# Kernel optimization log

Hardware: AMD Instinct MI355X
Metric: run time of the kernel (lower is better)

Reference implementation:

```python
import jax, jax.numpy as jnp
import numpy as np

DIM = 512
HEADS = 8
DIM_HEAD = 64
HIDDEN = HEADS * DIM_HEAD  # 512
SCALE = DIM_HEAD ** -0.5
EPS = 1e-12  # F.normalize default eps


def rms_norm(x, g):
    # F.normalize over channel dim (dim=1), then * g * sqrt(C)
    c = x.shape[1]
    norm = jnp.sqrt(jnp.sum(x * x, axis=1, keepdims=True))
    return x / jnp.maximum(norm, EPS) * g * (c ** 0.5)


def setup_inputs() -> dict:
    key = jax.random.key(0)
    ks = jax.random.split(key, 6)
    b, h, w = 16, 64, 64
    x = jax.random.normal(ks[0], (b, DIM, h, w), dtype=jnp.float32)
    g1 = jnp.ones((1, DIM, 1, 1), dtype=jnp.float32)
    # 1x1 conv weights stored as (out_ch, in_ch)
    Wqkv = jax.random.normal(ks[1], (HIDDEN * 3, DIM), dtype=jnp.float32) * (DIM ** -0.5)
    Wout = jax.random.normal(ks[2], (DIM, HIDDEN), dtype=jnp.float32) * (HIDDEN ** -0.5)
    bout = jax.random.normal(ks[3], (DIM,), dtype=jnp.float32) * 0.01
    g2 = jnp.ones((1, DIM, 1, 1), dtype=jnp.float32)
    return {"x": x, "g1": g1, "Wqkv": Wqkv, "Wout": Wout, "bout": bout, "g2": g2}


def reference(x, g1, Wqkv, Wout, bout, g2):
    b, c, h, w = x.shape
    n = h * w
    xn = rms_norm(x, g1)
    # 1x1 conv == channel matmul
    qkv = jnp.einsum('oc,bchw->bohw', Wqkv, xn)  # (b, 3*hidden, h, w)
    qkv = qkv.reshape(b, 3, HEADS, DIM_HEAD, n)
    q, k, v = qkv[:, 0], qkv[:, 1], qkv[:, 2]  # (b, heads, d, n)
    q = jax.nn.softmax(q, axis=-2) * SCALE      # softmax over feature dim
    k = jax.nn.softmax(k, axis=-1)               # softmax over spatial dim
    context = jnp.einsum('bhdn,bhen->bhde', k, v)  # (b,h,d,e) small
    out = jnp.einsum('bhde,bhdn->bhen', context, q)  # (b,h,e,n)
    out = out.reshape(b, HIDDEN, h, w)
    out = jnp.einsum('oc,bchw->bohw', Wout, out) + bout[None, :, None, None]
    return rms_norm(out, g2)
```

## Files before the change

kernel.cpp:

```cpp
#include <hip/hip_runtime.h>
#include <hip/hip_bf16.h>
#include <math.h>

#define B_ 16
#define C_ 512
#define N_ 4096
#define NCOL (B_ * N_)

typedef short bf16x8 __attribute__((ext_vector_type(8)));
typedef ushort ushort8_t __attribute__((ext_vector_type(8)));
typedef float f32x4 __attribute__((ext_vector_type(4)));

__device__ __forceinline__ ushort f2bf(float f) {
    unsigned u = __float_as_uint(f);
    unsigned r = (u + 0x7FFFu + ((u >> 16) & 1u)) >> 16;
    return (ushort)r;
}
__device__ __forceinline__ float bf2f(ushort u) {
    return __uint_as_float((unsigned)u << 16);
}
__device__ __forceinline__ void gload_lds16(const void* g, void* l) {
    __builtin_amdgcn_global_load_lds(
        (const __attribute__((address_space(1))) unsigned int*)g,
        (__attribute__((address_space(3))) unsigned int*)l, 16, 0, 0);
}

__global__ __launch_bounds__(256) void wprep2_k(const float* __restrict__ Wqkv,
                                                const float* __restrict__ g1,
                                                const float* __restrict__ Wout,
                                                ushort* __restrict__ Wqkvb,
                                                ushort* __restrict__ Woutb)
{
    int i = blockIdx.x * 256 + threadIdx.x;
    if (i < 196608) {
        float4 wv = reinterpret_cast<const float4*>(Wqkv)[i];
        const float4 gv = *reinterpret_cast<const float4*>(g1 + ((i * 4) & 511));
        ushort4 u;
        u.x = f2bf(wv.x * gv.x); u.y = f2bf(wv.y * gv.y);
        u.z = f2bf(wv.z * gv.z); u.w = f2bf(wv.w * gv.w);
        reinterpret_cast<ushort4*>(Wqkvb)[i] = u;
    } else {
        int j = i - 196608;
        float4 wv = reinterpret_cast<const float4*>(Wout)[j];
        ushort4 u;
        u.x = f2bf(wv.x); u.y = f2bf(wv.y); u.z = f2bf(wv.z); u.w = f2bf(wv.w);
        reinterpret_cast<ushort4*>(Woutb)[j] = u;
    }
}

__global__ __launch_bounds__(256) void transpose_k(const float* __restrict__ X,
                                                   ushort* __restrict__ Xt,
                                                   float* __restrict__ rs1)
{
    __shared__ float t[2][64][68];
    __shared__ float sr[16][64];
    const int b = blockIdx.y, n0 = blockIdx.x * 64;
    const int tid = threadIdx.x;
    const int tg = tid >> 4, tl = tid & 15;
    float sq[4] = {0.f, 0.f, 0.f, 0.f};
    for (int chunk = 0; chunk < 8; ++chunk) {
        const int buf = chunk & 1;
        const float* xp = X + ((size_t)b * C_ + chunk * 64) * N_ + n0;
        #pragma unroll
        for (int j = 0; j < 4; ++j) {
            int c = tg + j * 16;
            float4 v = *reinterpret_cast<const float4*>(xp + (size_t)c * N_ + tl * 4);
            *reinterpret_cast<float4*>(&t[buf][c][tl * 4]) = v;
            sq[0] += v.x * v.x; sq[1] += v.y * v.y;
            sq[2] += v.z * v.z; sq[3] += v.w * v.w;
        }
        __syncthreads();
        #pragma unroll
        for (int i = 0; i < 4; ++i) {
            int nl = tg + i * 16, cl = tl * 4;
            ushort4 u;
            u.x = f2bf(t[buf][cl + 0][nl]);
            u.y = f2bf(t[buf][cl + 1][nl]);
            u.z = f2bf(t[buf][cl + 2][nl]);
            u.w = f2bf(t[buf][cl + 3][nl]);
            *reinterpret_cast<ushort4*>(
                Xt + ((size_t)b * N_ + n0 + nl) * 512 + chunk * 64 + cl) = u;
        }
    }
    #pragma unroll
    for (int j = 0; j < 4; ++j) sr[tg][tl * 4 + j] = sq[j];
    __syncthreads();
    if (tid < 64) {
        float s = 0.f;
        #pragma unroll
        for (int g = 0; g < 16; ++g) s += sr[g][tid];
        rs1[(size_t)b * N_ + n0 + tid] = 22.627416998f / fmaxf(sqrtf(s), 1e-12f);
    }
}

__global__ __launch_bounds__(512, 2)
void mfma_gemm(const ushort* __restrict__ A, const ushort* __restrict__ Bt,
               const float* __restrict__ rs1,
               ushort* __restrict__ qT2, ushort* __restrict__ kd,
               ushort* __restrict__ vd)
{
    __shared__ __align__(16) char lds[2][2][32768];
    const int b  = blockIdx.z;
    const int n0 = blockIdx.x * 256;
    const int m0 = blockIdx.y * 256;
    const int tid = threadIdx.x;
    const int w = tid >> 6, l = tid & 63;
    const int wm = w >> 2, wn = w & 3;
    const int lq = l >> 4, lr = l & 15;
    const ushort* Bb = Bt + (size_t)b * N_ * 512;

    f32x4 acc[8][4];
    #pragma unroll
    for (int i = 0; i < 8; ++i)
        #pragma unroll
        for (int j = 0; j < 4; ++j)
            #pragma unroll
            for (int r = 0; r < 4; ++r) acc[i][j][r] = 0.f;

#define STAGE_STEP(t, i)                                                      \
    do {                                                                      \
        const int kb_ = (t) * 128;                                            \
        const int idx_ = (i) * 512 + tid;                                     \
        const int r_ = idx_ >> 3;                                             \
        const int ch_ = (idx_ & 7) ^ (r_ & 7);                                \
        gload_lds16((const char*)A + (size_t)(m0 + r_) * 1024 + kb_ + ch_ * 16,\
                    &lds[(t) & 1][0][idx_ * 16]);                             \
        gload_lds16((const char*)Bb + (size_t)(n0 + r_) * 1024 + kb_ + ch_ * 16,\
                    &lds[(t) & 1][1][idx_ * 16]);                             \
    } while (0)

    #pragma unroll
    for (int i = 0; i < 4; ++i) STAGE_STEP(0, i);

    bf16x8 bfr[4];
    #pragma unroll 2
    for (int t = 0; t < 8; ++t) {
        const char* As = lds[t & 1][0];
        const char* Bs = lds[t & 1][1];
        #pragma unroll
        for (int ph = 0; ph < 4; ++ph) {
            const int kk = ph >> 1, mg = ph & 1;
            bf16x8 af[4];
            if (ph != 0) {
                #pragma unroll
                for (int m2 = 0; m2 < 4; ++m2) {
                    int ra = wm * 128 + (mg * 4 + m2) * 16 + lr;
                    int ch = (kk * 4 + lq) ^ (ra & 7);
                    af[m2] = *(const bf16x8*)(As + ra * 128 + ch * 16);
                }
                if (mg == 0) {
                    #pragma unroll
                    for (int nf = 0; nf < 4; ++nf) {
                        int rb = wn * 64 + nf * 16 + lr;
                        int ch = (kk * 4 + lq) ^ (rb & 7);
                        bfr[nf] = *(const bf16x8*)(Bs + rb * 128 + ch * 16);
                    }
                }
            }
            if (t < 7) STAGE_STEP(t + 1, ph);
            if (ph == 0) {
                if (t < 7) { asm volatile("s_waitcnt vmcnt(2)" ::: "memory"); }
                else       { asm volatile("s_waitcnt vmcnt(0)" ::: "memory"); }
            }
            __builtin_amdgcn_s_barrier();
            if (ph == 0) {
                #pragma unroll
                for (int m2 = 0; m2 < 4; ++m2) {
                    int ra = wm * 128 + m2 * 16 + lr;
                    int ch = lq ^ (ra & 7);
                    af[m2] = *(const bf16x8*)(As + ra * 128 + ch * 16);
                }
                #pragma unroll
                for (int nf = 0; nf < 4; ++nf) {
                    int rb = wn * 64 + nf * 16 + lr;
                    int ch = lq ^ (rb & 7);
                    bfr[nf] = *(const bf16x8*)(Bs + rb * 128 + ch * 16);
                }
            }
            asm volatile("s_waitcnt lgkmcnt(0)" ::: "memory");
            __builtin_amdgcn_sched_barrier(0);
            __builtin_amdgcn_s_setprio(1);
            #pragma unroll
            for (int m2 = 0; m2 < 4; ++m2)
                #pragma unroll
                for (int nf = 0; nf < 4; ++nf)
                    acc[mg * 4 + m2][nf] = __builtin_amdgcn_mfma_f32_16x16x32_bf16(
                        af[m2], bfr[nf], acc[mg * 4 + m2][nf], 0, 0, 0);
            __builtin_amdgcn_s_setprio(0);
            __builtin_amdgcn_s_barrier();
        }
    }
#undef STAGE_STEP

    const int part = m0 >> 9;
    const int mloc = (m0 & 511) + wm * 128;
    const int nbase = n0 + wn * 64;
    if (part == 0) {
        #pragma unroll
        for (int hg = 0; hg < 2; ++hg) {
            const int head = (mloc >> 6) + hg;
            #pragma unroll
            for (int nf = 0; nf < 4; ++nf) {
                const int n = nbase + nf * 16 + lr;
                const float sc = rs1[(size_t)b * N_ + n];
                float v[4][4];
                float mx = -1e30f;
                #pragma unroll
                for (int m2 = 0; m2 < 4; ++m2)
                    #pragma unroll
                    for (int r = 0; r < 4; ++r) {
                        v[m2][r] = acc[hg * 4 + m2][nf][r] * sc;
                        mx = fmaxf(mx, v[m2][r]);
                    }
                mx = fmaxf(mx, __shfl_xor(mx, 16));
                mx = fmaxf(mx, __shfl_xor(mx, 32));
                float s = 0.f;
                #pragma unroll
                for (int m2 = 0; m2 < 4; ++m2)
                    #pragma unroll
                    for (int r = 0; r < 4; ++r) {
                        v[m2][r] = __expf(v[m2][r] - mx);
                        s += v[m2][r];
                    }
                s += __shfl_xor(s, 16);
                s += __shfl_xor(s, 32);
                const float r8 = 0.125f / s;
                ushort* qp = qT2 + ((size_t)b * N_ + n) * 512 + head * 64;
                #pragma unroll
                for (int m2 = 0; m2 < 4; ++m2) {
                    ushort4 u;
                    u.x = f2bf(v[m2][0] * r8);
                    u.y = f2bf(v[m2][1] * r8);
                    u.z = f2bf(v[m2][2] * r8);
                    u.w = f2bf(v[m2][3] * r8);
                    *reinterpret_cast<ushort4*>(qp + m2 * 16 + lq * 4) = u;
                }
            }
        }
    } else {
        ushort* dst = (part == 1) ? kd : vd;
        #pragma unroll
        for (int nf = 0; nf < 4; ++nf) {
            const int n = nbase + nf * 16 + lr;
            const float sc = rs1[(size_t)b * N_ + n];
            #pragma unroll
            for (int mf = 0; mf < 8; ++mf) {
                const int o = mloc + mf * 16 + lq * 4;
                #pragma unroll
                for (int r = 0; r < 4; ++r)
                    dst[((size_t)b * 512 + o + r) * N_ + n] =
                        f2bf(acc[mf][nf][r] * sc);
            }
        }
    }
}

__global__ __launch_bounds__(256) void rowstat_k(const ushort* __restrict__ kk,
                                                 float* __restrict__ rowm,
                                                 float* __restrict__ rowr)
{
    const int row = blockIdx.x * 4 + (threadIdx.x >> 6);
    const int lane = threadIdx.x & 63;
    const ushort* p = kk + (size_t)row * N_;
    float vals[64];
    #pragma unroll
    for (int j = 0; j < 8; ++j) {
        ushort8_t u = *reinterpret_cast<const ushort8_t*>(p + lane * 8 + j * 512);
        #pragma unroll
        for (int t = 0; t < 8; ++t) vals[j * 8 + t] = bf2f(u[t]);
    }
    float mx = -1e30f;
    #pragma unroll
    for (int i = 0; i < 64; ++i) mx = fmaxf(mx, vals[i]);
    #pragma unroll
    for (int o = 32; o >= 1; o >>= 1) mx = fmaxf(mx, __shfl_xor(mx, o));
    float s = 0.f;
    #pragma unroll
    for (int i = 0; i < 64; ++i) s += __expf(vals[i] - mx);
    #pragma unroll
    for (int o = 32; o >= 1; o >>= 1) s += __shfl_xor(s, o);
    if (lane == 0) { rowm[row] = mx; rowr[row] = 1.f / s; }
}

__global__ __launch_bounds__(256) void ctx_k(const ushort* __restrict__ kk,
                                             const ushort* __restrict__ vv,
                                             const float* __restrict__ rowm,
                                             const float* __restrict__ rowr,
                                             float* __restrict__ ctxp)
{
    const int bh = blockIdx.x, chunk = blockIdx.y;
    const ushort* kp = kk + (size_t)bh * 64 * N_;
    const ushort* vp = vv + (size_t)bh * 64 * N_;
    __shared__ __align__(16) ushort kx[64 * 128];
    __shared__ __align__(16) ushort vx[64 * 128];
    __shared__ float rm[64];
    const int tid = threadIdx.x;
    const int w = tid >> 6, l = tid & 63;
    const int lq = l >> 4, lr = l & 15;
    const int we = w >> 1, wd = w & 1;
    if (tid < 64) rm[tid] = rowm[(size_t)bh * 64 + tid];
    __syncthreads();

    f32x4 acc[2][2];
    #pragma unroll
    for (int i = 0; i < 2; ++i)
        #pragma unroll
        for (int j = 0; j < 2; ++j)
            #pragma unroll
            for (int r = 0; r < 4; ++r) acc[i][j][r] = 0.f;

    for (int s = 0; s < 8; ++s) {
        const int n0 = chunk * 1024 + s * 128;
        #pragma unroll
        for (int i = 0; i < 4; ++i) {
            int idx = i * 256 + tid;
            int row = idx >> 4;
            int ch  = (idx & 15) ^ (row & 15);
            gload_lds16((const char*)(vp + (size_t)row * N_ + n0 + ch * 8),
                        (char*)vx + idx * 16);
        }
        #pragma unroll
        for (int i = 0; i < 4; ++i) {
            int idx = i * 256 + tid;
            int row = idx >> 4;
            int ch  = idx & 15;
            ushort8_t u = *reinterpret_cast<const ushort8_t*>(
                kp + (size_t)row * N_ + n0 + ch * 8);
            float m_ = rm[row];
            ushort8_t o;
            #pragma unroll
            for (int t = 0; t < 8; ++t) o[t] = f2bf(__expf(bf2f(u[t]) - m_));
            *(ushort8_t*)((char*)kx + (row * 16 + (ch ^ (row & 15))) * 16) = o;
        }
        __syncthreads();
        #pragma unroll
        for (int k2 = 0; k2 < 4; ++k2) {
            bf16x8 af[2], bfr[2];
            #pragma unroll
            for (int i = 0; i < 2; ++i) {
                int re = we * 32 + i * 16 + lr;
                int cha = (k2 * 4 + lq) ^ (re & 15);
                af[i] = *(const bf16x8*)((const char*)vx + (re * 16 + cha) * 16);
                int rd = wd * 32 + i * 16 + lr;
                int chb = (k2 * 4 + lq) ^ (rd & 15);
                bfr[i] = *(const bf16x8*)((const char*)kx + (rd * 16 + chb) * 16);
            }
            #pragma unroll
            for (int i = 0; i < 2; ++i)
                #pragma unroll
                for (int j = 0; j < 2; ++j)
                    acc[i][j] = __builtin_amdgcn_mfma_f32_16x16x32_bf16(
                        af[i], bfr[j], acc[i][j], 0, 0, 0);
        }
        __syncthreads();
    }
    float* cbase = ctxp + ((size_t)bh * 4 + chunk) * 4096;
    #pragma unroll
    for (int j = 0; j < 2; ++j) {
        const int d = wd * 32 + j * 16 + lr;
        const float rr = rowr[(size_t)bh * 64 + d];
        #pragma unroll
        for (int i = 0; i < 2; ++i) {
            const int e0 = we * 32 + i * 16 + lq * 4;
            float4 wv;
            wv.x = acc[i][j][0] * rr;
            wv.y = acc[i][j][1] * rr;
            wv.z = acc[i][j][2] * rr;
            wv.w = acc[i][j][3] * rr;
            *reinterpret_cast<float4*>(cbase + (size_t)d * 64 + e0) = wv;
        }
    }
}

__global__ __launch_bounds__(256) void wcbuild_k(const ushort* __restrict__ Wb,
                                                 const float* __restrict__ ctxp,
                                                 ushort* __restrict__ Wc)
{
    const int oh = blockIdx.x, h = blockIdx.y, b = blockIdx.z;
    const int bh = b * 8 + h;
    __shared__ __align__(16) ushort ws[256 * 64];
    __shared__ __align__(16) ushort cs[64 * 64];
    const int tid = threadIdx.x;
    const int w = tid >> 6, l = tid & 63;
    const int lq = l >> 4, lr = l & 15;

    #pragma unroll
    for (int i = 0; i < 8; ++i) {
        int idx = i * 256 + tid;
        int row = idx >> 3;
        int ch = (idx & 7) ^ (row & 7);
        gload_lds16(Wb + (size_t)(oh * 256 + row) * 512 + h * 64 + ch * 8,
                    (char*)ws + idx * 16);
    }
    {
        const float* cp = ctxp + (size_t)bh * 4 * 4096;
        const int d = tid >> 2, eb = (tid & 3) * 16;
        float vs[16];
        #pragma unroll
        for (int t4 = 0; t4 < 4; ++t4) {
            float4 a0 = *(const float4*)(cp + d * 64 + eb + t4 * 4);
            float4 a1 = *(const float4*)(cp + 4096 + d * 64 + eb + t4 * 4);
            float4 a2 = *(const float4*)(cp + 8192 + d * 64 + eb + t4 * 4);
            float4 a3 = *(const float4*)(cp + 12288 + d * 64 + eb + t4 * 4);
            vs[t4 * 4 + 0] = a0.x + a1.x + a2.x + a3.x;
            vs[t4 * 4 + 1] = a0.y + a1.y + a2.y + a3.y;
            vs[t4 * 4 + 2] = a0.z + a1.z + a2.z + a3.z;
            vs[t4 * 4 + 3] = a0.w + a1.w + a2.w + a3.w;
        }
        ushort8_t o0, o1;
        #pragma unroll
        for (int t = 0; t < 8; ++t) { o0[t] = f2bf(vs[t]); o1[t] = f2bf(vs[8 + t]); }
        const int c0 = (eb >> 3) ^ (d & 7);
        const int c1 = ((eb >> 3) + 1) ^ (d & 7);
        *(ushort8_t*)((char*)cs + (d * 8 + c0) * 16) = o0;
        *(ushort8_t*)((char*)cs + (d * 8 + c1) * 16) = o1;
    }
    __syncthreads();

    f32x4 acc[4][4];
    #pragma unroll
    for (int i = 0; i < 4; ++i)
        #pragma unroll
        for (int j = 0; j < 4; ++j)
            #pragma unroll
            for (int r = 0; r < 4; ++r) acc[i][j][r] = 0.f;

    #pragma unroll
    for (int kk = 0; kk < 2; ++kk) {
        bf16x8 af[4], bfr[4];
        #pragma unroll
        for (int mf = 0; mf < 4; ++mf) {
            int ra = w * 64 + mf * 16 + lr;
            int ch = (kk * 4 + lq) ^ (ra & 7);
            af[mf] = *(const bf16x8*)((const char*)ws + (ra * 8 + ch) * 16);
        }
        #pragma unroll
        for (int nf = 0; nf < 4; ++nf) {
            int rd = nf * 16 + lr;
            int ch = (kk * 4 + lq) ^ (rd & 7);
            bfr[nf] = *(const bf16x8*)((const char*)cs + (rd * 8 + ch) * 16);
        }
        #pragma unroll
        for (int mf = 0; mf < 4; ++mf)
            #pragma unroll
            for (int nf = 0; nf < 4; ++nf)
                acc[mf][nf] = __builtin_amdgcn_mfma_f32_16x16x32_bf16(
                    af[mf], bfr[nf], acc[mf][nf], 0, 0, 0);
    }

    ushort* wp = Wc + (size_t)b * 262144 + h * 64;
    #pragma unroll
    for (int mf = 0; mf < 4; ++mf)
        #pragma unroll
        for (int r = 0; r < 4; ++r) {
            const int o = oh * 256 + w * 64 + mf * 16 + lq * 4 + r;
            #pragma unroll
            for (int nf = 0; nf < 4; ++nf)
                wp[(size_t)o * 512 + nf * 16 + lr] = f2bf(acc[mf][nf][r]);
        }
}

__global__ __launch_bounds__(512, 2)
void gemm2_k(const ushort* __restrict__ Wc,
             const ushort* __restrict__ Bt,
             const float* __restrict__ bias,
             const float* __restrict__ g2,
             float* __restrict__ outp)
{
    __shared__ __align__(16) ushort As[512 * 64];
    __shared__ __align__(16) ushort Bs[128 * 64];
    const int b  = blockIdx.y;
    const int n0 = blockIdx.x * 128;
    const int tid = threadIdx.x;
    const int w = tid >> 6, l = tid & 63;
    const int lq = l >> 4, lr = l & 15;
    const ushort* A  = Wc + (size_t)b * 262144;
    const ushort* Bb = Bt + (size_t)b * N_ * 512;

    f32x4 acc[4][8];
    #pragma unroll
    for (int i = 0; i < 4; ++i)
        #pragma unroll
        for (int j = 0; j < 8; ++j)
            #pragma unroll
            for (int r = 0; r < 4; ++r) acc[i][j][r] = 0.f;

    for (int k0 = 0; k0 < 512; k0 += 64) {
        #pragma unroll
        for (int i = 0; i < 8; ++i) {
            int base = i * 512 + w * 64;
            int idx = base + l;
            int r = idx >> 3, ch = (idx & 7) ^ (r & 7);
            gload_lds16((const char*)A + (size_t)r * 1024 + k0 * 2 + ch * 16,
                        (char*)As + (size_t)base * 16);
        }
        #pragma unroll
        for (int i = 0; i < 2; ++i) {
            int base = i * 512 + w * 64;
            int idx = base + l;
            int r = idx >> 3, ch = (idx & 7) ^ (r & 7);
            gload_lds16((const char*)Bb + (size_t)(n0 + r) * 1024 + k0 * 2 + ch * 16,
                        (char*)Bs + (size_t)base * 16);
        }
        __syncthreads();
        #pragma unroll
        for (int kk = 0; kk < 2; ++kk) {
            bf16x8 af[4], bfv[8];
            #pragma unroll
            for (int mf = 0; mf < 4; ++mf) {
                int ra = w * 64 + mf * 16 + lr;
                int ch = (kk * 4 + lq) ^ (ra & 7);
                af[mf] = *(const bf16x8*)((const char*)As + ra * 128 + ch * 16);
            }
            #pragma unroll
            for (int nf = 0; nf < 8; ++nf) {
                int rb = nf * 16 + lr;
                int ch = (kk * 4 + lq) ^ (rb & 7);
                bfv[nf] = *(const bf16x8*)((const char*)Bs + rb * 128 + ch * 16);
            }
            #pragma unroll
            for (int mf = 0; mf < 4; ++mf)
                #pragma unroll
                for (int nf = 0; nf < 8; ++nf)
                    acc[mf][nf] = __builtin_amdgcn_mfma_f32_16x16x32_bf16(
                        af[mf], bfv[nf], acc[mf][nf], 0, 0, 0);
        }
        __syncthreads();
    }

    float4 bv[4], g2v[4];
    #pragma unroll
    for (int mf = 0; mf < 4; ++mf) {
        bv[mf]  = *reinterpret_cast<const float4*>(bias + w * 64 + mf * 16 + lq * 4);
        g2v[mf] = *reinterpret_cast<const float4*>(g2   + w * 64 + mf * 16 + lq * 4);
    }
    float csq[8] = {};
    #pragma unroll
    for (int mf = 0; mf < 4; ++mf)
        #pragma unroll
        for (int nf = 0; nf < 8; ++nf)
            #pragma unroll
            for (int r = 0; r < 4; ++r) {
                float wv = acc[mf][nf][r] + ((const float*)&bv[mf])[r];
                acc[mf][nf][r] = wv;
                csq[nf] += wv * wv;
            }
    #pragma unroll
    for (int nf = 0; nf < 8; ++nf) {
        csq[nf] += __shfl_xor(csq[nf], 16);
        csq[nf] += __shfl_xor(csq[nf], 32);
    }
    float* red  = (float*)As;
    float* rs2s = red + 1024;
    if (lq == 0) {
        #pragma unroll
        for (int nf = 0; nf < 8; ++nf)
            red[w * 128 + nf * 16 + lr] = csq[nf];
    }
    __syncthreads();
    if (tid < 128) {
        float s = 0.f;
        #pragma unroll
        for (int j = 0; j < 8; ++j) s += red[j * 128 + tid];
        rs2s[tid] = 22.627416998f / fmaxf(sqrtf(s), 1e-12f);
    }
    __syncthreads();
    #pragma unroll
    for (int nf = 0; nf < 8; ++nf) {
        const float rsv = rs2s[nf * 16 + lr];
        const int n = n0 + nf * 16 + lr;
        #pragma unroll
        for (int mf = 0; mf < 4; ++mf) {
            const int o = w * 64 + mf * 16 + lq * 4;
            float* p = outp + ((size_t)b * 512 + o) * N_ + n;
            #pragma unroll
            for (int r = 0; r < 4; ++r)
                p[(size_t)r * N_] = acc[mf][nf][r] * rsv * ((const float*)&g2v[mf])[r];
        }
    }
}

extern "C" void kernel_launch(void* const* d_in, const int* in_sizes, int n_in,
                              void* d_out, int out_size, void* d_ws, size_t ws_size,
                              hipStream_t stream)
{
    const float* x    = (const float*)d_in[0];
    const float* g1   = (const float*)d_in[1];
    const float* Wqkv = (const float*)d_in[2];
    const float* Wout = (const float*)d_in[3];
    const float* bout = (const float*)d_in[4];
    const float* g2   = (const float*)d_in[5];
    float* out = (float*)d_out;

    char* wsb = (char*)d_ws;
    ushort* qbuf  = (ushort*)wsb;
    ushort* kbuf  = (ushort*)(wsb + ((size_t)64 << 20));
    ushort* vbuf  = (ushort*)(wsb + ((size_t)128 << 20));
    ushort* Xt    = (ushort*)(wsb + ((size_t)192 << 20));
    float*  ctxp  = (float*)Xt;
    float*  rowm  = (float*)(wsb + ((size_t)200 << 20));
    float*  rowr  = rowm + 8192;
    ushort* Wcb   = (ushort*)(wsb + ((size_t)201 << 20));
    char*   tail  = wsb + ((size_t)256 << 20);
    ushort* Wqkvb = (ushort*)tail;
    ushort* Woutb = (ushort*)(tail + (size_t)1536 * 512 * 2);
    float*  rs1   = (float*)(tail + (size_t)1536 * 512 * 2 + (size_t)512 * 512 * 2);

    wprep2_k<<<1024, 256, 0, stream>>>(Wqkv, g1, Wout, Wqkvb, Woutb);
    transpose_k<<<dim3(64, 16), 256, 0, stream>>>(x, Xt, rs1);
    mfma_gemm<<<dim3(16, 6, B_), 512, 0, stream>>>(Wqkvb, Xt, rs1,
                                                   qbuf, kbuf, vbuf);
    rowstat_k<<<2048, 256, 0, stream>>>(kbuf, rowm, rowr);
    ctx_k<<<dim3(B_ * 8, 4), 256, 0, stream>>>(kbuf, vbuf, rowm, rowr, ctxp);
    wcbuild_k<<<dim3(2, 8, B_), 256, 0, stream>>>(Woutb, ctxp, Wcb);
    gemm2_k<<<dim3(32, B_), 512, 0, stream>>>(Wcb, qbuf, bout, g2, out);
}
```

Baseline: 305.1 us.

## Fuse key softmax row statistics into QKV GEMM epilogue with partial merge

The QKV GEMM epilogue now computes per-tile partial max and sum-of-exp for each key row from the accumulators and writes them to workspace. A small merge kernel then combines the 64 partials per row, replacing the rowstat pass that re-read the whole bf16 key buffer. This removes a full read of the K tensor but adds shuffle reductions and exps to the GEMM epilogue. The stats come from fp32 values rather than the rounded bf16 keys. The new path is taken only when the workspace is large enough, otherwise it falls back to rowstat.

```diff
diff --git a/kernel.cpp b/kernel.cpp
--- a/kernel.cpp
+++ b/kernel.cpp
@@ -97,7 +97,8 @@
 void mfma_gemm(const ushort* __restrict__ A, const ushort* __restrict__ Bt,
                const float* __restrict__ rs1,
                ushort* __restrict__ qT2, ushort* __restrict__ kd,
-               ushort* __restrict__ vd)
+               ushort* __restrict__ vd,
+               float* __restrict__ kpm, float* __restrict__ kps)
 {
     __shared__ __align__(16) char lds[2][2][32768];
     const int b  = blockIdx.z;
@@ -239,20 +240,71 @@
         }
     } else {
         ushort* dst = (part == 1) ? kd : vd;
+        float sc4[4];
+        #pragma unroll
+        for (int nf = 0; nf < 4; ++nf)
+            sc4[nf] = rs1[(size_t)b * N_ + nbase + nf * 16 + lr];
         #pragma unroll
         for (int nf = 0; nf < 4; ++nf) {
             const int n = nbase + nf * 16 + lr;
-            const float sc = rs1[(size_t)b * N_ + n];
             #pragma unroll
             for (int mf = 0; mf < 8; ++mf) {
                 const int o = mloc + mf * 16 + lq * 4;
                 #pragma unroll
                 for (int r = 0; r < 4; ++r)
                     dst[((size_t)b * 512 + o + r) * N_ + n] =
-                        f2bf(acc[mf][nf][r] * sc);
-            }
-        }
-    }
+                        f2bf(acc[mf][nf][r] * sc4[nf]);
+            }
+        }
+        if (part == 1 && kpm) {
+            const int p = blockIdx.x * 4 + wn;
+            #pragma unroll
+            for (int mf = 0; mf < 8; ++mf)
+                #pragma unroll
+                for (int r = 0; r < 4; ++r) {
+                    float v0 = acc[mf][0][r] * sc4[0];
+                    float v1 = acc[mf][1][r] * sc4[1];
+                    float v2 = acc[mf][2][r] * sc4[2];
+                    float v3 = acc[mf][3][r] * sc4[3];
+                    float m = fmaxf(fmaxf(v0, v1), fmaxf(v2, v3));
+                    m = fmaxf(m, __shfl_xor(m, 1));
+                    m = fmaxf(m, __shfl_xor(m, 2));
+                    m = fmaxf(m, __shfl_xor(m, 4));
+                    m = fmaxf(m, __shfl_xor(m, 8));
+                    float s = __expf(v0 - m) + __expf(v1 - m)
+                            + __expf(v2 - m) + __expf(v3 - m);
+                    s += __shfl_xor(s, 1);
+                    s += __shfl_xor(s, 2);
+                    s += __shfl_xor(s, 4);
+                    s += __shfl_xor(s, 8);
+                    if (lr == 0) {
+                        const int dk = mloc + mf * 16 + lq * 4 + r;
+                        kpm[((size_t)p * B_ + b) * 512 + dk] = m;
+                        kps[((size_t)p * B_ + b) * 512 + dk] = s;
+                    }
+                }
+        }
+    }
+}
+
+__global__ __launch_bounds__(256) void kstat_merge_k(const float* __restrict__ kpm,
+                                                     const float* __restrict__ kps,
+                                                     float* __restrict__ rowm,
+                                                     float* __restrict__ rowr)
+{
+    int idx = blockIdx.x * 256 + threadIdx.x;
+    int b = idx >> 9, dk = idx & 511;
+    float m = -1e30f;
+    #pragma unroll 8
+    for (int p = 0; p < 64; ++p)
+        m = fmaxf(m, kpm[((size_t)p * B_ + b) * 512 + dk]);
+    float s = 0.f;
+    #pragma unroll 8
+    for (int p = 0; p < 64; ++p)
+        s += kps[((size_t)p * B_ + b) * 512 + dk] *
+             __expf(kpm[((size_t)p * B_ + b) * 512 + dk] - m);
+    rowm[idx] = m;
+    rowr[idx] = 1.f / s;
 }
 
 __global__ __launch_bounds__(256) void rowstat_k(const ushort* __restrict__ kk,
@@ -605,12 +657,18 @@
     ushort* Wqkvb = (ushort*)tail;
     ushort* Woutb = (ushort*)(tail + (size_t)1536 * 512 * 2);
     float*  rs1   = (float*)(tail + (size_t)1536 * 512 * 2 + (size_t)512 * 512 * 2);
+    const bool fused_stats = ws_size >= ((size_t)263 << 20);
+    float* kpm = fused_stats ? (float*)(wsb + ((size_t)259 << 20)) : nullptr;
+    float* kps = fused_stats ? (float*)(wsb + ((size_t)261 << 20)) : nullptr;
 
     wprep2_k<<<1024, 256, 0, stream>>>(Wqkv, g1, Wout, Wqkvb, Woutb);
     transpose_k<<<dim3(64, 16), 256, 0, stream>>>(x, Xt, rs1);
     mfma_gemm<<<dim3(16, 6, B_), 512, 0, stream>>>(Wqkvb, Xt, rs1,
-                                                   qbuf, kbuf, vbuf);
-    rowstat_k<<<2048, 256, 0, stream>>>(kbuf, rowm, rowr);
+                                                   qbuf, kbuf, vbuf, kpm, kps);
+    if (fused_stats)
+        kstat_merge_k<<<32, 256, 0, stream>>>(kpm, kps, rowm, rowr);
+    else
+        rowstat_k<<<2048, 256, 0, stream>>>(kbuf, rowm, rowr);
     ctx_k<<<dim3(B_ * 8, 4), 256, 0, stream>>>(kbuf, vbuf, rowm, rowr, ctxp);
     wcbuild_k<<<dim3(2, 8, B_), 256, 0, stream>>>(Woutb, ctxp, Wcb);
     gemm2_k<<<dim3(32, B_), 512, 0, stream>>>(Wcb, qbuf, bout, g2, out);
```

Result: slower. 386.8 us (+26.8%).

## Fuse k-softmax statistics into context kernel, drop max subtraction

Applied to the files above, without the earlier changes.

Removes the separate rowstat kernel that computed the per-row max and sum for the spatial softmax of k. The context kernel now exponentiates k directly without subtracting the max, accumulates per-row partial sums per chunk, and writes them out. The wcbuild kernel combines the four chunk sums and applies the reciprocal when reducing the context partials. This saves one full read of the k buffer and a launch, but exp without the max shift can overflow if k values grow large.

```diff
diff --git a/kernel.cpp b/kernel.cpp
--- a/kernel.cpp
+++ b/kernel.cpp
@@ -255,51 +255,20 @@
     }
 }
 
-__global__ __launch_bounds__(256) void rowstat_k(const ushort* __restrict__ kk,
-                                                 float* __restrict__ rowm,
-                                                 float* __restrict__ rowr)
-{
-    const int row = blockIdx.x * 4 + (threadIdx.x >> 6);
-    const int lane = threadIdx.x & 63;
-    const ushort* p = kk + (size_t)row * N_;
-    float vals[64];
-    #pragma unroll
-    for (int j = 0; j < 8; ++j) {
-        ushort8_t u = *reinterpret_cast<const ushort8_t*>(p + lane * 8 + j * 512);
-        #pragma unroll
-        for (int t = 0; t < 8; ++t) vals[j * 8 + t] = bf2f(u[t]);
-    }
-    float mx = -1e30f;
-    #pragma unroll
-    for (int i = 0; i < 64; ++i) mx = fmaxf(mx, vals[i]);
-    #pragma unroll
-    for (int o = 32; o >= 1; o >>= 1) mx = fmaxf(mx, __shfl_xor(mx, o));
-    float s = 0.f;
-    #pragma unroll
-    for (int i = 0; i < 64; ++i) s += __expf(vals[i] - mx);
-    #pragma unroll
-    for (int o = 32; o >= 1; o >>= 1) s += __shfl_xor(s, o);
-    if (lane == 0) { rowm[row] = mx; rowr[row] = 1.f / s; }
-}
-
 __global__ __launch_bounds__(256) void ctx_k(const ushort* __restrict__ kk,
                                              const ushort* __restrict__ vv,
-                                             const float* __restrict__ rowm,
-                                             const float* __restrict__ rowr,
-                                             float* __restrict__ ctxp)
+                                             float* __restrict__ ctxp,
+                                             float* __restrict__ srowp)
 {
     const int bh = blockIdx.x, chunk = blockIdx.y;
     const ushort* kp = kk + (size_t)bh * 64 * N_;
     const ushort* vp = vv + (size_t)bh * 64 * N_;
     __shared__ __align__(16) ushort kx[64 * 128];
     __shared__ __align__(16) ushort vx[64 * 128];
-    __shared__ float rm[64];
     const int tid = threadIdx.x;
     const int w = tid >> 6, l = tid & 63;
     const int lq = l >> 4, lr = l & 15;
     const int we = w >> 1, wd = w & 1;
-    if (tid < 64) rm[tid] = rowm[(size_t)bh * 64 + tid];
-    __syncthreads();
 
     f32x4 acc[2][2];
     #pragma unroll
@@ -308,6 +277,8 @@
         for (int j = 0; j < 2; ++j)
             #pragma unroll
             for (int r = 0; r < 4; ++r) acc[i][j][r] = 0.f;
+
+    float se[4] = {0.f, 0.f, 0.f, 0.f};
 
     for (int s = 0; s < 8; ++s) {
         const int n0 = chunk * 1024 + s * 128;
@@ -326,10 +297,15 @@
             int ch  = idx & 15;
             ushort8_t u = *reinterpret_cast<const ushort8_t*>(
                 kp + (size_t)row * N_ + n0 + ch * 8);
-            float m_ = rm[row];
             ushort8_t o;
-            #pragma unroll
-            for (int t = 0; t < 8; ++t) o[t] = f2bf(__expf(bf2f(u[t]) - m_));
+            float ss = 0.f;
+            #pragma unroll
+            for (int t = 0; t < 8; ++t) {
+                float e = __expf(bf2f(u[t]));
+                ss += e;
+                o[t] = f2bf(e);
+            }
+            se[i] += ss;
             *(ushort8_t*)((char*)kx + (row * 16 + (ch ^ (row & 15))) * 16) = o;
         }
         __syncthreads();
@@ -354,19 +330,32 @@
         }
         __syncthreads();
     }
+
+    #pragma unroll
+    for (int i = 0; i < 4; ++i) {
+        float v = se[i];
+        v += __shfl_xor(v, 1);
+        v += __shfl_xor(v, 2);
+        v += __shfl_xor(v, 4);
+        v += __shfl_xor(v, 8);
+        if (lr == 0) {
+            const int row = i * 16 + w * 4 + lq;
+            srowp[((size_t)bh * 4 + chunk) * 64 + row] = v;
+        }
+    }
+
     float* cbase = ctxp + ((size_t)bh * 4 + chunk) * 4096;
     #pragma unroll
     for (int j = 0; j < 2; ++j) {
         const int d = wd * 32 + j * 16 + lr;
-        const float rr = rowr[(size_t)bh * 64 + d];
         #pragma unroll
         for (int i = 0; i < 2; ++i) {
             const int e0 = we * 32 + i * 16 + lq * 4;
             float4 wv;
-            wv.x = acc[i][j][0] * rr;
-            wv.y = acc[i][j][1] * rr;
-            wv.z = acc[i][j][2] * rr;
-            wv.w = acc[i][j][3] * rr;
+            wv.x = acc[i][j][0];
+            wv.y = acc[i][j][1];
+            wv.z = acc[i][j][2];
+            wv.w = acc[i][j][3];
             *reinterpret_cast<float4*>(cbase + (size_t)d * 64 + e0) = wv;
         }
     }
@@ -374,6 +363,7 @@
 
 __global__ __launch_bounds__(256) void wcbuild_k(const ushort* __restrict__ Wb,
                                                  const float* __restrict__ ctxp,
+                                                 const float* __restrict__ srowp,
                                                  ushort* __restrict__ Wc)
 {
     const int oh = blockIdx.x, h = blockIdx.y, b = blockIdx.z;
@@ -394,7 +384,9 @@
     }
     {
         const float* cp = ctxp + (size_t)bh * 4 * 4096;
+        const float* sp = srowp + (size_t)bh * 4 * 64;
         const int d = tid >> 2, eb = (tid & 3) * 16;
+        const float rinv = 1.f / (sp[d] + sp[64 + d] + sp[128 + d] + sp[192 + d]);
         float vs[16];
         #pragma unroll
         for (int t4 = 0; t4 < 4; ++t4) {
@@ -402,10 +394,10 @@
             float4 a1 = *(const float4*)(cp + 4096 + d * 64 + eb + t4 * 4);
             float4 a2 = *(const float4*)(cp + 8192 + d * 64 + eb + t4 * 4);
             float4 a3 = *(const float4*)(cp + 12288 + d * 64 + eb + t4 * 4);
-            vs[t4 * 4 + 0] = a0.x + a1.x + a2.x + a3.x;
-            vs[t4 * 4 + 1] = a0.y + a1.y + a2.y + a3.y;
-            vs[t4 * 4 + 2] = a0.z + a1.z + a2.z + a3.z;
-            vs[t4 * 4 + 3] = a0.w + a1.w + a2.w + a3.w;
+            vs[t4 * 4 + 0] = (a0.x + a1.x + a2.x + a3.x) * rinv;
+            vs[t4 * 4 + 1] = (a0.y + a1.y + a2.y + a3.y) * rinv;
+            vs[t4 * 4 + 2] = (a0.z + a1.z + a2.z + a3.z) * rinv;
+            vs[t4 * 4 + 3] = (a0.w + a1.w + a2.w + a3.w) * rinv;
         }
         ushort8_t o0, o1;
         #pragma unroll
@@ -598,8 +590,7 @@
     ushort* vbuf  = (ushort*)(wsb + ((size_t)128 << 20));
     ushort* Xt    = (ushort*)(wsb + ((size_t)192 << 20));
     float*  ctxp  = (float*)Xt;
-    float*  rowm  = (float*)(wsb + ((size_t)200 << 20));
-    float*  rowr  = rowm + 8192;
+    float*  srowp = (float*)(wsb + ((size_t)200 << 20));
     ushort* Wcb   = (ushort*)(wsb + ((size_t)201 << 20));
     char*   tail  = wsb + ((size_t)256 << 20);
     ushort* Wqkvb = (ushort*)tail;
@@ -610,8 +601,7 @@
     transpose_k<<<dim3(64, 16), 256, 0, stream>>>(x, Xt, rs1);
     mfma_gemm<<<dim3(16, 6, B_), 512, 0, stream>>>(Wqkvb, Xt, rs1,
                                                    qbuf, kbuf, vbuf);
-    rowstat_k<<<2048, 256, 0, stream>>>(kbuf, rowm, rowr);
-    ctx_k<<<dim3(B_ * 8, 4), 256, 0, stream>>>(kbuf, vbuf, rowm, rowr, ctxp);
-    wcbuild_k<<<dim3(2, 8, B_), 256, 0, stream>>>(Woutb, ctxp, Wcb);
+    ctx_k<<<dim3(B_ * 8, 4), 256, 0, stream>>>(kbuf, vbuf, ctxp, srowp);
+    wcbuild_k<<<dim3(2, 8, B_), 256, 0, stream>>>(Woutb, ctxp, srowp, Wcb);
     gemm2_k<<<dim3(32, B_), 512, 0, stream>>>(Wcb, qbuf, bout, g2, out);
 }
```

Measured after the change: 292.9 us (median of 2 runs). 1.04x faster.
